# Kernel optimization log

Hardware: AMD Instinct MI355X
Metric: run time of the kernel (lower is better)

Reference implementation:

```python
import jax, jax.numpy as jnp
import numpy as np

B, CIN, F, H, W = 4, 256, 128, 64, 64
EPS = 1e-5

def _conv1x1(x, Wm, b):
    # x: [B,C,H,W], Wm: [O,C] (1x1 conv kernel), b: [O]
    return jnp.einsum('bchw,oc->bohw', x, Wm) + b[None, :, None, None]

def setup_inputs() -> dict:
    key = jax.random.key(0)
    ks = jax.random.split(key, 11)
    s_in = 1.0 / np.sqrt(CIN)
    s_f = 1.0 / np.sqrt(F)
    return {
        'x':    jax.random.normal(ks[0], (B, CIN, H, W), jnp.float32),
        'Wg':   jax.random.normal(ks[1], (F, CIN), jnp.float32) * s_in,
        'bg':   jax.random.normal(ks[2], (F,), jnp.float32) * s_in,
        'Wt':   jax.random.normal(ks[3], (F, CIN), jnp.float32) * s_in,
        'bt':   jax.random.normal(ks[4], (F,), jnp.float32) * s_in,
        'Wp':   jax.random.normal(ks[5], (F, CIN), jnp.float32) * s_in,
        'bp':   jax.random.normal(ks[6], (F,), jnp.float32) * s_in,
        'Wz':   jax.random.normal(ks[7], (CIN, F), jnp.float32) * s_f,
        'bz':   jax.random.normal(ks[8], (CIN,), jnp.float32) * s_f,
        'ln_w': jax.random.normal(ks[9], (CIN, H, W), jnp.float32) * 0.1,
        'ln_b': jax.random.normal(ks[10], (CIN, H, W), jnp.float32) * 0.1,
    }

def reference(x, Wg, bg, Wt, bt, Wp, bp, Wz, bz, ln_w, ln_b):
    b, _, h, w = x.shape
    n = h * w
    # 1x1 conv projections
    g = _conv1x1(x, Wg, bg).reshape(b, F, n).transpose(0, 2, 1)      # [B,N,F]
    theta = _conv1x1(x, Wt, bt).reshape(b, F, n).transpose(0, 2, 1)  # [B,N,F]
    phi = _conv1x1(x, Wp, bp).reshape(b, F, n)                        # [B,F,N]
    # embedded-Gaussian affinity + softmax attention
    f = jnp.einsum('bnf,bfm->bnm', theta, phi)                        # [B,N,N]
    attn = jax.nn.softmax(f, axis=-1)
    y = jnp.einsum('bnm,bmf->bnf', attn, g)                           # [B,N,F]
    y = y.transpose(0, 2, 1).reshape(b, F, h, w)                      # [B,F,H,W]
    # output projection
    z = _conv1x1(y, Wz, bz)                                           # [B,CIN,H,W]
    # LayerNorm over (C,H,W) per sample, affine params shaped [C,H,W]
    mu = jnp.mean(z, axis=(1, 2, 3), keepdims=True)
    var = jnp.var(z, axis=(1, 2, 3), keepdims=True)
    z = (z - mu) * jax.lax.rsqrt(var + EPS)
    z = z * ln_w[None] + ln_b[None]
    return z + x
```

## Files before the change

### kernel.cpp

```cpp
#include <hip/hip_runtime.h>
#include <stdint.h>

#define CIN 256
#define FDIM 128
#define NSP 4096
#define EPS 1e-5f

typedef __attribute__((ext_vector_type(8))) short short8;
typedef __attribute__((ext_vector_type(4))) float f32x4;
typedef __attribute__((ext_vector_type(16))) float f32x16;

__device__ __forceinline__ short f2bf(float f) {
  union { float f; uint32_t u; } v; v.f = f;
  uint32_t r = v.u + 0x7fffu + ((v.u >> 16) & 1u);
  return (short)(r >> 16);
}
__device__ __forceinline__ float bf2f(short h) {
  union { uint32_t u; float f; } v; v.u = ((uint32_t)(uint16_t)h) << 16;
  return v.f;
}

__global__ void prep_weights(const float* __restrict__ Wg, const float* __restrict__ Wt,
                             const float* __restrict__ Wp, const float* __restrict__ Wz,
                             short* __restrict__ Wbf, short* __restrict__ Wzbf) {
  int idx = blockIdx.x * 256 + threadIdx.x;
  if (idx < 384 * 256) {
    int row = idx >> 8, col = idx & 255;
    float v;
    if (row < 128)       v = Wt[row * 256 + col];
    else if (row < 256)  v = Wp[(row - 128) * 256 + col];
    else                 v = Wg[(row - 256) * 256 + col];
    Wbf[idx] = f2bf(v);
  } else {
    int j = idx - 384 * 256;
    if (j < 256 * 128) Wzbf[j] = f2bf(Wz[j]);
  }
}

__global__ void prep_xT(const float* __restrict__ x, short* __restrict__ xT) {
  __shared__ float tile[32][33];
  int b = blockIdx.z, c0 = blockIdx.y * 32, n0 = blockIdx.x * 32;
  int r = threadIdx.x >> 5, c = threadIdx.x & 31;
  const float* xb = x + (size_t)b * CIN * NSP;
#pragma unroll
  for (int k = 0; k < 4; k++)
    tile[r + 8 * k][c] = xb[(size_t)(c0 + r + 8 * k) * NSP + n0 + c];
  __syncthreads();
  short* xTb = xT + (size_t)b * NSP * CIN;
#pragma unroll
  for (int k = 0; k < 4; k++)
    xTb[(size_t)(n0 + r + 8 * k) * CIN + c0 + c] = f2bf(tile[c][r + 8 * k]);
}

__global__ void __launch_bounds__(256)
proj_kernel(const short* __restrict__ xT, const short* __restrict__ Wbf,
            const float* __restrict__ bt, const float* __restrict__ bp,
            const float* __restrict__ bg,
            short* __restrict__ theta, short* __restrict__ Kb, short* __restrict__ gT) {
  __shared__ short lds[5120];
  int bx = blockIdx.x;
  int b = bx >> 7;
  int n0 = (bx & 127) << 5;
  int p = blockIdx.y;
  int t = threadIdx.x, w = t >> 6, lane = t & 63, l15 = lane & 15, quad = lane >> 4;

  const short* arow = xT + (size_t)(b * NSP + n0 + (w & 1) * 16 + l15) * CIN;
  short8 a[8];
#pragma unroll
  for (int s = 0; s < 8; s++) a[s] = *(const short8*)(arow + s * 32 + quad * 8);

  const short* Wsrc = Wbf + p * 128 * 256;
  f32x4 zero = {0.f, 0.f, 0.f, 0.f};
  f32x4 acc[4];
#pragma unroll
  for (int i = 0; i < 4; i++) acc[i] = zero;

#pragma unroll
  for (int s = 0; s < 8; s++) {
#pragma unroll
    for (int ft = 0; ft < 4; ft++) {
      int ftg = (w >> 1) * 4 + ft;
      short8 bfr = *(const short8*)(Wsrc + (ftg * 16 + l15) * 256 + s * 32 + quad * 8);
      acc[ft] = __builtin_amdgcn_mfma_f32_16x16x32_bf16(a[s], bfr, acc[ft], 0, 0, 0);
    }
  }

  const float* bias = (p == 0) ? bt : (p == 1) ? bp : bg;
  if (p < 2) {
#pragma unroll
    for (int ft = 0; ft < 4; ft++) {
      int ftg = (w >> 1) * 4 + ft;
      float bv = bias[ftg * 16 + l15];
#pragma unroll
      for (int rr = 0; rr < 4; rr++) {
        int n = (w & 1) * 16 + quad * 4 + rr;
        lds[n * 136 + ftg * 16 + l15] = f2bf(acc[ft][rr] + bv);
      }
    }
    __syncthreads();
    short* dst = ((p == 0) ? theta : Kb) + (size_t)(b * NSP + n0) * FDIM;
#pragma unroll
    for (int i = 0; i < 2; i++) {
      int flat = t + 256 * i;
      int row = flat >> 4, ch = flat & 15;
      *(short8*)(dst + (size_t)row * FDIM + ch * 8) = *(const short8*)(lds + row * 136 + ch * 8);
    }
  } else {
#pragma unroll
    for (int ft = 0; ft < 4; ft++) {
      int ftg = (w >> 1) * 4 + ft;
      float bv = bias[ftg * 16 + l15];
#pragma unroll
      for (int rr = 0; rr < 4; rr++) {
        int n = (w & 1) * 16 + quad * 4 + rr;
        lds[(ftg * 16 + l15) * 40 + n] = f2bf(acc[ft][rr] + bv);
      }
    }
    __syncthreads();
    short* dst = gT + (size_t)b * FDIM * NSP + n0;
#pragma unroll
    for (int i = 0; i < 2; i++) {
      int flat = t + 256 * i;
      int f = flat >> 2, c = flat & 3;
      *(short8*)(dst + (size_t)f * NSP + c * 8) = *(const short8*)(lds + f * 40 + c * 8);
    }
  }
}

__global__ void __launch_bounds__(256, 2)
flash_kernel(const short* __restrict__ thetab, const short* __restrict__ Kb,
             const short* __restrict__ gT, short* __restrict__ opart,
             float* __restrict__ lpart) {
  __shared__ __attribute__((aligned(16))) char smem[37888];

  const int bx = blockIdx.x;
  const int b  = bx >> 7;
  const int r  = bx & 127;
  const int q0 = (r >> 2) << 7;
  const int kc = r & 3;
  const int t = threadIdx.x, w = t >> 6, lane = t & 63;
  const int l31 = lane & 31, h = lane >> 5;
  const int qw = q0 + w * 32;

  const short* Qsrc = thetab + (size_t)b * NSP * FDIM;
  const short* Ksrc = Kb + (size_t)b * NSP * FDIM;
  const short* Vsrc = gT + (size_t)b * FDIM * NSP;

  short8 qf[8];
#pragma unroll
  for (int s = 0; s < 8; s++)
    qf[s] = *(const short8*)(Qsrc + (size_t)(qw + l31) * FDIM + s * 16 + h * 8);

  f32x16 O[4];
#pragma unroll
  for (int i = 0; i < 4; i++)
#pragma unroll
    for (int j = 0; j < 16; j++) O[i][j] = 0.f;
  float lsum = 0.f;

  const int kr0 = t >> 4, kcc0 = t & 15;
  const int kr1 = 16 + (t >> 4);
  const int vf0 = t >> 2, vcc0 = t & 3;
  const int vf1 = 64 + (t >> 2);

  const int kA0 = kc << 10;
  short8 rK0, rK1, rV0, rV1;

  {
    rK0 = *(const short8*)(Ksrc + (size_t)(kA0 + kr0) * FDIM + kcc0 * 8);
    rK1 = *(const short8*)(Ksrc + (size_t)(kA0 + kr1) * FDIM + kcc0 * 8);
    rV0 = *(const short8*)(Vsrc + (size_t)vf0 * NSP + kA0 + vcc0 * 8);
    rV1 = *(const short8*)(Vsrc + (size_t)vf1 * NSP + kA0 + vcc0 * 8);
    short* Kd = (short*)(smem);
    short* Vd = (short*)(smem + 8704);
    *(short8*)(Kd + kr0 * 136 + kcc0 * 8) = rK0;
    *(short8*)(Kd + kr1 * 136 + kcc0 * 8) = rK1;
    *(short8*)(Vd + vf0 * 40 + vcc0 * 8) = rV0;
    *(short8*)(Vd + vf1 * 40 + vcc0 * 8) = rV1;
  }

#pragma unroll 2
  for (int it = 0; it < 32; ++it) {
    __syncthreads();
    if (it < 31) {
      int kk = kA0 + (it + 1) * 32;
      rK0 = *(const short8*)(Ksrc + (size_t)(kk + kr0) * FDIM + kcc0 * 8);
      rK1 = *(const short8*)(Ksrc + (size_t)(kk + kr1) * FDIM + kcc0 * 8);
      rV0 = *(const short8*)(Vsrc + (size_t)vf0 * NSP + kk + vcc0 * 8);
      rV1 = *(const short8*)(Vsrc + (size_t)vf1 * NSP + kk + vcc0 * 8);
    }
    const short* Kl = (const short*)(smem + (it & 1) * 18944);
    const short* Vl = (const short*)(smem + (it & 1) * 18944 + 8704);

    f32x16 S;
#pragma unroll
    for (int j = 0; j < 16; j++) S[j] = 0.f;
    __builtin_amdgcn_s_setprio(1);
#pragma unroll
    for (int s = 0; s < 8; s++) {
      short8 ak = *(const short8*)(Kl + l31 * 136 + s * 16 + h * 8);
      S = __builtin_amdgcn_mfma_f32_32x32x16_bf16(ak, qf[s], S, 0, 0, 0);
    }
    __builtin_amdgcn_s_setprio(0);

    float p[16];
#pragma unroll
    for (int i = 0; i < 16; i++) p[i] = __expf(S[i]);
    float t8[8];
#pragma unroll
    for (int i = 0; i < 8; i++) t8[i] = p[2 * i] + p[2 * i + 1];
    lsum += ((t8[0] + t8[1]) + (t8[2] + t8[3])) + ((t8[4] + t8[5]) + (t8[6] + t8[7]));

    short8 Af[2];
#pragma unroll
    for (int tt = 0; tt < 2; tt++) {
      const int rb = tt * 8;
      short8 af;
#pragma unroll
      for (int rr = 0; rr < 4; rr++) {
        float qv = h ? p[rb + rr] : p[rb + 4 + rr];
        float wv = __shfl_xor(qv, 32, 64);
        float e0 = h ? wv : p[rb + rr];
        float e1 = h ? p[rb + 4 + rr] : wv;
        af[rr] = f2bf(e0);
        af[4 + rr] = f2bf(e1);
      }
      Af[tt] = af;
    }

    __builtin_amdgcn_s_setprio(1);
#pragma unroll
    for (int ft = 0; ft < 4; ft++) {
#pragma unroll
      for (int tt = 0; tt < 2; tt++) {
        short8 bv = *(const short8*)(Vl + (ft * 32 + l31) * 40 + tt * 16 + h * 8);
        O[ft] = __builtin_amdgcn_mfma_f32_32x32x16_bf16(Af[tt], bv, O[ft], 0, 0, 0);
      }
    }
    __builtin_amdgcn_s_setprio(0);

    if (it < 31) {
      short* Kd = (short*)(smem + ((it + 1) & 1) * 18944);
      short* Vd = (short*)(smem + ((it + 1) & 1) * 18944 + 8704);
      *(short8*)(Kd + kr0 * 136 + kcc0 * 8) = rK0;
      *(short8*)(Kd + kr1 * 136 + kcc0 * 8) = rK1;
      *(short8*)(Vd + vf0 * 40 + vcc0 * 8) = rV0;
      *(short8*)(Vd + vf1 * 40 + vcc0 * 8) = rV1;
    }
  }

  lsum += __shfl_xor(lsum, 32, 64);

  __syncthreads();
  short* tr = (short*)smem + w * 32 * 136;
#pragma unroll
  for (int ft = 0; ft < 4; ft++) {
#pragma unroll
    for (int reg = 0; reg < 16; reg++) {
      int rowq = (reg & 3) + 8 * (reg >> 2) + 4 * h;
      tr[rowq * 136 + ft * 32 + l31] = f2bf(O[ft][reg]);
    }
  }
  short* od = opart + ((size_t)(kc * 4 + b) * NSP + qw) * FDIM;
#pragma unroll
  for (int i = 0; i < 8; i++) {
    int slot = lane + 64 * i;
    int row = slot >> 4, c = slot & 15;
    *(short8*)(od + (size_t)row * FDIM + c * 8) = *(const short8*)(tr + row * 136 + c * 8);
  }
  if (h == 0) lpart[(size_t)(kc * 4 + b) * NSP + qw + l31] = lsum;
}

__global__ void __launch_bounds__(256)
zproj_kernel(const short* __restrict__ opart, const float* __restrict__ lpart,
             const short* __restrict__ Wzbf, const float* __restrict__ bz,
             short* __restrict__ zb, float* __restrict__ psums) {
  __shared__ short ldsT[128 * 40];
  __shared__ float wsum[4][2];
  int bx = blockIdx.x;
  int b = bx >> 7;
  int n0 = (bx & 127) << 5;
  int ch0 = blockIdx.y * 128;
  int t = threadIdx.x, w = t >> 6, lane = t & 63, l15 = lane & 15, quad = lane >> 4;

  int row = n0 + (w & 1) * 16 + l15;
  float L = 0.f;
#pragma unroll
  for (int kcc = 0; kcc < 4; kcc++) L += lpart[(size_t)(kcc * 4 + b) * NSP + row];
  float inv = 1.0f / L;

  short8 a[4];
#pragma unroll
  for (int s = 0; s < 4; s++) {
    float accv[8] = {0, 0, 0, 0, 0, 0, 0, 0};
#pragma unroll
    for (int kcc = 0; kcc < 4; kcc++) {
      short8 v = *(const short8*)(opart + ((size_t)(kcc * 4 + b) * NSP + row) * FDIM + s * 32 + quad * 8);
#pragma unroll
      for (int j = 0; j < 8; j++) accv[j] += bf2f(v[j]);
    }
    short8 av;
#pragma unroll
    for (int j = 0; j < 8; j++) av[j] = f2bf(accv[j] * inv);
    a[s] = av;
  }

  f32x4 zero = {0.f, 0.f, 0.f, 0.f};
  f32x4 acc[4];
#pragma unroll
  for (int i = 0; i < 4; i++) acc[i] = zero;
#pragma unroll
  for (int s = 0; s < 4; s++) {
#pragma unroll
    for (int ct = 0; ct < 4; ct++) {
      int co = ch0 + (w >> 1) * 64 + ct * 16 + l15;
      short8 bfr = *(const short8*)(Wzbf + (size_t)co * FDIM + s * 32 + quad * 8);
      acc[ct] = __builtin_amdgcn_mfma_f32_16x16x32_bf16(a[s], bfr, acc[ct], 0, 0, 0);
    }
  }

  float s1 = 0.0f, s2 = 0.0f;
#pragma unroll
  for (int ct = 0; ct < 4; ct++) {
    int cg = (w >> 1) * 64 + ct * 16 + l15;
    float bv = bz[ch0 + cg];
#pragma unroll
    for (int rr = 0; rr < 4; rr++) {
      float v = acc[ct][rr] + bv;
      s1 += v; s2 += v * v;
      ldsT[cg * 40 + (w & 1) * 16 + quad * 4 + rr] = f2bf(v);
    }
  }
#pragma unroll
  for (int off = 32; off >= 1; off >>= 1) {
    s1 += __shfl_xor(s1, off, 64);
    s2 += __shfl_xor(s2, off, 64);
  }
  if (lane == 0) { wsum[w][0] = s1; wsum[w][1] = s2; }
  __syncthreads();
  if (t == 0) {
    int bid = blockIdx.y * 512 + bx;
    psums[bid * 2] = wsum[0][0] + wsum[1][0] + wsum[2][0] + wsum[3][0];
    psums[bid * 2 + 1] = wsum[0][1] + wsum[1][1] + wsum[2][1] + wsum[3][1];
  }
  short* dst = zb + (size_t)b * CIN * NSP + (size_t)ch0 * NSP + n0;
#pragma unroll
  for (int i = 0; i < 2; i++) {
    int flat = t + 256 * i;
    int c = flat >> 2, ch = flat & 3;
    *(short8*)(dst + (size_t)c * NSP + ch * 8) = *(const short8*)(ldsT + c * 40 + ch * 8);
  }
}

__global__ void reduce_sums(const float* __restrict__ psums, float* __restrict__ sums) {
  __shared__ float red[8];
  int t = threadIdx.x;
  if (t < 8) red[t] = 0.f;
  __syncthreads();
  for (int i = t; i < 1024; i += 256) {
    int b = (i & 511) >> 7;
    atomicAdd(&red[b * 2], psums[i * 2]);
    atomicAdd(&red[b * 2 + 1], psums[i * 2 + 1]);
  }
  __syncthreads();
  if (t < 8) sums[t] = red[t];
}

__global__ void __launch_bounds__(256)
finalize_kernel(const short* __restrict__ zbuf, const float* __restrict__ x,
                const float* __restrict__ lnw, const float* __restrict__ lnb,
                const float* __restrict__ sums, float* __restrict__ out) {
  int gid = blockIdx.x * 256 + threadIdx.x;
  size_t e0 = (size_t)gid * 8;
  int b = (int)(e0 >> 20);
  size_t ib = e0 & ((size_t)(1u << 20) - 1);
  float mean = sums[b * 2] * (1.0f / 1048576.0f);
  float var = sums[b * 2 + 1] * (1.0f / 1048576.0f) - mean * mean;
  float rs = rsqrtf(var + EPS);
  short8 zv = *(const short8*)(zbuf + e0);
#pragma unroll
  for (int k = 0; k < 8; k++) {
    float z = bf2f(zv[k]);
    out[e0 + k] = (z - mean) * rs * lnw[ib + k] + lnb[ib + k] + x[e0 + k];
  }
}

extern "C" void kernel_launch(void* const* d_in, const int* in_sizes, int n_in,
                              void* d_out, int out_size, void* d_ws, size_t ws_size,
                              hipStream_t stream) {
  const float* x   = (const float*)d_in[0];
  const float* Wg  = (const float*)d_in[1];
  const float* bg  = (const float*)d_in[2];
  const float* Wt  = (const float*)d_in[3];
  const float* bt  = (const float*)d_in[4];
  const float* Wp  = (const float*)d_in[5];
  const float* bp  = (const float*)d_in[6];
  const float* Wz  = (const float*)d_in[7];
  const float* bz  = (const float*)d_in[8];
  const float* lnw = (const float*)d_in[9];
  const float* lnb = (const float*)d_in[10];
  float* out = (float*)d_out;

  char* ws = (char*)d_ws;
  short* Wbf    = (short*)(ws);
  short* Wzbf   = (short*)(ws + 196608);
  short* xT     = (short*)(ws + 262144);
  short* opart  = (short*)(ws + 262144);
  float* lpart  = (float*)(ws + 17039360);
  short* thetab = (short*)(ws + 17301504);
  short* Kb     = (short*)(ws + 21495808);
  short* gT     = (short*)(ws + 25690112);
  short* zb     = (short*)(ws + 17301504);
  float* sums   = (float*)(ws + 29884416);
  float* psums  = (float*)(ws + 29884448);

  prep_weights<<<512, 256, 0, stream>>>(Wg, Wt, Wp, Wz, Wbf, Wzbf);
  prep_xT<<<dim3(128, 8, 4), 256, 0, stream>>>(x, xT);
  proj_kernel<<<dim3(512, 3), 256, 0, stream>>>(xT, Wbf, bt, bp, bg, thetab, Kb, gT);
  flash_kernel<<<512, 256, 0, stream>>>(thetab, Kb, gT, opart, lpart);
  zproj_kernel<<<dim3(512, 2), 256, 0, stream>>>(opart, lpart, Wzbf, bz, zb, psums);
  reduce_sums<<<1, 256, 0, stream>>>(psums, sums);
  finalize_kernel<<<2048, 256, 0, stream>>>(zb, x, lnw, lnb, sums, out);
}
```

Before: 198.4 us.

## Process 64-key tiles per iteration and use packed bf16 convert with permlane swap

Doubles the key/value tile per loop iteration from 32 to 64 keys, halving the number of barriers and loop iterations, and computes two independent score tiles so their MFMA chains can interleave. It also replaces the scalar bf16 rounding and shuffle-based lane exchange with v_cvt_pk_bf16_f32 and v_permlane32_swap_b32 inline assembly. LDS use doubles to about 74 KB per block and more prefetch registers are live, which may reduce occupancy under the launch bound of 2 blocks per CU.

```diff
diff --git a/kernel.cpp b/kernel.cpp
--- a/kernel.cpp
+++ b/kernel.cpp
@@ -131,7 +131,7 @@
 flash_kernel(const short* __restrict__ thetab, const short* __restrict__ Kb,
              const short* __restrict__ gT, short* __restrict__ opart,
              float* __restrict__ lpart) {
-  __shared__ __attribute__((aligned(16))) char smem[37888];
+  __shared__ __attribute__((aligned(16))) char smem[75776];
 
   const int bx = blockIdx.x;
   const int b  = bx >> 7;
@@ -164,88 +164,117 @@
   const int vf1 = 64 + (t >> 2);
 
   const int kA0 = kc << 10;
-  short8 rK0, rK1, rV0, rV1;
+  short8 rKa0, rKa1, rKb0, rKb1, rVa0, rVa1, rVb0, rVb1;
 
   {
-    rK0 = *(const short8*)(Ksrc + (size_t)(kA0 + kr0) * FDIM + kcc0 * 8);
-    rK1 = *(const short8*)(Ksrc + (size_t)(kA0 + kr1) * FDIM + kcc0 * 8);
-    rV0 = *(const short8*)(Vsrc + (size_t)vf0 * NSP + kA0 + vcc0 * 8);
-    rV1 = *(const short8*)(Vsrc + (size_t)vf1 * NSP + kA0 + vcc0 * 8);
-    short* Kd = (short*)(smem);
-    short* Vd = (short*)(smem + 8704);
-    *(short8*)(Kd + kr0 * 136 + kcc0 * 8) = rK0;
-    *(short8*)(Kd + kr1 * 136 + kcc0 * 8) = rK1;
-    *(short8*)(Vd + vf0 * 40 + vcc0 * 8) = rV0;
-    *(short8*)(Vd + vf1 * 40 + vcc0 * 8) = rV1;
+    rKa0 = *(const short8*)(Ksrc + (size_t)(kA0 + kr0) * FDIM + kcc0 * 8);
+    rKa1 = *(const short8*)(Ksrc + (size_t)(kA0 + kr1) * FDIM + kcc0 * 8);
+    rKb0 = *(const short8*)(Ksrc + (size_t)(kA0 + 32 + kr0) * FDIM + kcc0 * 8);
+    rKb1 = *(const short8*)(Ksrc + (size_t)(kA0 + 32 + kr1) * FDIM + kcc0 * 8);
+    rVa0 = *(const short8*)(Vsrc + (size_t)vf0 * NSP + kA0 + vcc0 * 8);
+    rVa1 = *(const short8*)(Vsrc + (size_t)vf1 * NSP + kA0 + vcc0 * 8);
+    rVb0 = *(const short8*)(Vsrc + (size_t)vf0 * NSP + kA0 + 32 + vcc0 * 8);
+    rVb1 = *(const short8*)(Vsrc + (size_t)vf1 * NSP + kA0 + 32 + vcc0 * 8);
+    short* Ka = (short*)(smem);
+    short* Kbd = (short*)(smem + 8704);
+    short* Va = (short*)(smem + 17408);
+    short* Vb = (short*)(smem + 27648);
+    *(short8*)(Ka + kr0 * 136 + kcc0 * 8) = rKa0;
+    *(short8*)(Ka + kr1 * 136 + kcc0 * 8) = rKa1;
+    *(short8*)(Kbd + kr0 * 136 + kcc0 * 8) = rKb0;
+    *(short8*)(Kbd + kr1 * 136 + kcc0 * 8) = rKb1;
+    *(short8*)(Va + vf0 * 40 + vcc0 * 8) = rVa0;
+    *(short8*)(Va + vf1 * 40 + vcc0 * 8) = rVa1;
+    *(short8*)(Vb + vf0 * 40 + vcc0 * 8) = rVb0;
+    *(short8*)(Vb + vf1 * 40 + vcc0 * 8) = rVb1;
   }
 
 #pragma unroll 2
-  for (int it = 0; it < 32; ++it) {
+  for (int it = 0; it < 16; ++it) {
     __syncthreads();
-    if (it < 31) {
-      int kk = kA0 + (it + 1) * 32;
-      rK0 = *(const short8*)(Ksrc + (size_t)(kk + kr0) * FDIM + kcc0 * 8);
-      rK1 = *(const short8*)(Ksrc + (size_t)(kk + kr1) * FDIM + kcc0 * 8);
-      rV0 = *(const short8*)(Vsrc + (size_t)vf0 * NSP + kk + vcc0 * 8);
-      rV1 = *(const short8*)(Vsrc + (size_t)vf1 * NSP + kk + vcc0 * 8);
-    }
-    const short* Kl = (const short*)(smem + (it & 1) * 18944);
-    const short* Vl = (const short*)(smem + (it & 1) * 18944 + 8704);
-
-    f32x16 S;
-#pragma unroll
-    for (int j = 0; j < 16; j++) S[j] = 0.f;
+    if (it < 15) {
+      int kk = kA0 + (it + 1) * 64;
+      rKa0 = *(const short8*)(Ksrc + (size_t)(kk + kr0) * FDIM + kcc0 * 8);
+      rKa1 = *(const short8*)(Ksrc + (size_t)(kk + kr1) * FDIM + kcc0 * 8);
+      rKb0 = *(const short8*)(Ksrc + (size_t)(kk + 32 + kr0) * FDIM + kcc0 * 8);
+      rKb1 = *(const short8*)(Ksrc + (size_t)(kk + 32 + kr1) * FDIM + kcc0 * 8);
+      rVa0 = *(const short8*)(Vsrc + (size_t)vf0 * NSP + kk + vcc0 * 8);
+      rVa1 = *(const short8*)(Vsrc + (size_t)vf1 * NSP + kk + vcc0 * 8);
+      rVb0 = *(const short8*)(Vsrc + (size_t)vf0 * NSP + kk + 32 + vcc0 * 8);
+      rVb1 = *(const short8*)(Vsrc + (size_t)vf1 * NSP + kk + 32 + vcc0 * 8);
+    }
+    const char* bufc = smem + (it & 1) * 37888;
+    const short* Kla = (const short*)(bufc);
+    const short* Klb = (const short*)(bufc + 8704);
+    const short* Vla = (const short*)(bufc + 17408);
+    const short* Vlb = (const short*)(bufc + 27648);
+
+    f32x16 S0, S1;
+#pragma unroll
+    for (int j = 0; j < 16; j++) { S0[j] = 0.f; S1[j] = 0.f; }
     __builtin_amdgcn_s_setprio(1);
 #pragma unroll
     for (int s = 0; s < 8; s++) {
-      short8 ak = *(const short8*)(Kl + l31 * 136 + s * 16 + h * 8);
-      S = __builtin_amdgcn_mfma_f32_32x32x16_bf16(ak, qf[s], S, 0, 0, 0);
+      short8 ak0 = *(const short8*)(Kla + l31 * 136 + s * 16 + h * 8);
+      short8 ak1 = *(const short8*)(Klb + l31 * 136 + s * 16 + h * 8);
+      S0 = __builtin_amdgcn_mfma_f32_32x32x16_bf16(ak0, qf[s], S0, 0, 0, 0);
+      S1 = __builtin_amdgcn_mfma_f32_32x32x16_bf16(ak1, qf[s], S1, 0, 0, 0);
     }
     __builtin_amdgcn_s_setprio(0);
 
-    float p[16];
-#pragma unroll
-    for (int i = 0; i < 16; i++) p[i] = __expf(S[i]);
-    float t8[8];
-#pragma unroll
-    for (int i = 0; i < 8; i++) t8[i] = p[2 * i] + p[2 * i + 1];
-    lsum += ((t8[0] + t8[1]) + (t8[2] + t8[3])) + ((t8[4] + t8[5]) + (t8[6] + t8[7]));
-
-    short8 Af[2];
-#pragma unroll
-    for (int tt = 0; tt < 2; tt++) {
-      const int rb = tt * 8;
-      short8 af;
-#pragma unroll
-      for (int rr = 0; rr < 4; rr++) {
-        float qv = h ? p[rb + rr] : p[rb + 4 + rr];
-        float wv = __shfl_xor(qv, 32, 64);
-        float e0 = h ? wv : p[rb + rr];
-        float e1 = h ? p[rb + 4 + rr] : wv;
-        af[rr] = f2bf(e0);
-        af[4 + rr] = f2bf(e1);
+    short8 AfA[2], AfB[2];
+#pragma unroll
+    for (int sub = 0; sub < 2; sub++) {
+      float p[16];
+#pragma unroll
+      for (int i = 0; i < 16; i++) p[i] = __expf(sub ? S1[i] : S0[i]);
+      float t8[8];
+#pragma unroll
+      for (int i = 0; i < 8; i++) t8[i] = p[2 * i] + p[2 * i + 1];
+      lsum += ((t8[0] + t8[1]) + (t8[2] + t8[3])) + ((t8[4] + t8[5]) + (t8[6] + t8[7]));
+
+      uint32_t W[8];
+#pragma unroll
+      for (int j = 0; j < 8; j++)
+        asm("v_cvt_pk_bf16_f32 %0, %1, %2" : "=v"(W[j]) : "v"(p[2 * j]), "v"(p[2 * j + 1]));
+      asm("v_permlane32_swap_b32 %0, %1" : "+v"(W[0]), "+v"(W[2]));
+      asm("v_permlane32_swap_b32 %0, %1" : "+v"(W[1]), "+v"(W[3]));
+      asm("v_permlane32_swap_b32 %0, %1" : "+v"(W[4]), "+v"(W[6]));
+      asm("v_permlane32_swap_b32 %0, %1" : "+v"(W[5]), "+v"(W[7]));
+      union { short8 s; uint32_t u[4]; } u0, u1;
+      u0.u[0] = W[0]; u0.u[1] = W[1]; u0.u[2] = W[2]; u0.u[3] = W[3];
+      u1.u[0] = W[4]; u1.u[1] = W[5]; u1.u[2] = W[6]; u1.u[3] = W[7];
+      if (sub) { AfB[0] = u0.s; AfB[1] = u1.s; }
+      else     { AfA[0] = u0.s; AfA[1] = u1.s; }
+    }
+
+    __builtin_amdgcn_s_setprio(1);
+#pragma unroll
+    for (int ft = 0; ft < 4; ft++) {
+#pragma unroll
+      for (int tt = 0; tt < 2; tt++) {
+        short8 bva = *(const short8*)(Vla + (ft * 32 + l31) * 40 + tt * 16 + h * 8);
+        O[ft] = __builtin_amdgcn_mfma_f32_32x32x16_bf16(AfA[tt], bva, O[ft], 0, 0, 0);
+        short8 bvb = *(const short8*)(Vlb + (ft * 32 + l31) * 40 + tt * 16 + h * 8);
+        O[ft] = __builtin_amdgcn_mfma_f32_32x32x16_bf16(AfB[tt], bvb, O[ft], 0, 0, 0);
       }
-      Af[tt] = af;
-    }
-
-    __builtin_amdgcn_s_setprio(1);
-#pragma unroll
-    for (int ft = 0; ft < 4; ft++) {
-#pragma unroll
-      for (int tt = 0; tt < 2; tt++) {
-        short8 bv = *(const short8*)(Vl + (ft * 32 + l31) * 40 + tt * 16 + h * 8);
-        O[ft] = __builtin_amdgcn_mfma_f32_32x32x16_bf16(Af[tt], bv, O[ft], 0, 0, 0);
-      }
     }
     __builtin_amdgcn_s_setprio(0);
 
-    if (it < 31) {
-      short* Kd = (short*)(smem + ((it + 1) & 1) * 18944);
-      short* Vd = (short*)(smem + ((it + 1) & 1) * 18944 + 8704);
-      *(short8*)(Kd + kr0 * 136 + kcc0 * 8) = rK0;
-      *(short8*)(Kd + kr1 * 136 + kcc0 * 8) = rK1;
-      *(short8*)(Vd + vf0 * 40 + vcc0 * 8) = rV0;
-      *(short8*)(Vd + vf1 * 40 + vcc0 * 8) = rV1;
+    if (it < 15) {
+      char* nb = smem + ((it + 1) & 1) * 37888;
+      short* Ka = (short*)(nb);
+      short* Kbd = (short*)(nb + 8704);
+      short* Va = (short*)(nb + 17408);
+      short* Vb = (short*)(nb + 27648);
+      *(short8*)(Ka + kr0 * 136 + kcc0 * 8) = rKa0;
+      *(short8*)(Ka + kr1 * 136 + kcc0 * 8) = rKa1;
+      *(short8*)(Kbd + kr0 * 136 + kcc0 * 8) = rKb0;
+      *(short8*)(Kbd + kr1 * 136 + kcc0 * 8) = rKb1;
+      *(short8*)(Va + vf0 * 40 + vcc0 * 8) = rVa0;
+      *(short8*)(Va + vf1 * 40 + vcc0 * 8) = rVa1;
+      *(short8*)(Vb + vf0 * 40 + vcc0 * 8) = rVb0;
+      *(short8*)(Vb + vf1 * 40 + vcc0 * 8) = rVb1;
     }
   }
 
```

Result: faster. 193.4 us (-2.5%).
